# Optimization experiments

Hardware: AMD Instinct MI355X
Metric: run time of the kernel (lower is better)

## Reference

```python
import jax, jax.numpy as jnp
import numpy as np


def setup_inputs() -> dict:
    key = jax.random.key(0)
    k1, k2 = jax.random.split(key)
    q, k, d5 = 128, 2048, 768
    return {
        "tgt": jax.random.normal(k1, (q, d5), dtype=jnp.float32),
        "memory": jax.random.normal(k2, (k, d5), dtype=jnp.float32),
        "seq_len": 32,
    }


def reference(tgt, memory, seq_len):
    q, d5 = tgt.shape
    k, _ = memory.shape
    z = d5 // seq_len  # per-token sub-dim
    query_t = tgt.reshape(q, seq_len, z)    # [q, t, d]
    key_m = memory.reshape(k, seq_len, z)   # [k, s, d]
    # Full late-interaction similarity tensor [q, k, s, t]
    score = jnp.einsum('qtd,ksd->qkst', query_t, key_m)
    # max over memory tokens (s) and over query tokens (t), concat, mean
    pooled = jnp.concatenate((score.max(axis=2), score.max(axis=3)), axis=-1)  # [q, k, 2*seq_len]
    score_p = jax.nn.sigmoid(pooled.mean(axis=-1))  # [q, k]
    return (score_p, score_p)
```

## Files before the change

kernel.cpp:

```cpp
#include <hip/hip_runtime.h>
#include <hip/hip_bf16.h>

typedef __bf16 bf16x8 __attribute__((ext_vector_type(8)));
typedef float  f32x16 __attribute__((ext_vector_type(16)));

constexpr int QN  = 128;
constexpr int KN  = 2048;
constexpr int D5  = 768;
constexpr int SL  = 32;
constexpr int ZD  = 24;
constexpr int KCH = 16;

static __device__ __forceinline__ float max3f(float a, float b, float c) {
    return fmaxf(fmaxf(a, b), c);
}

static __device__ __forceinline__ float redmax16(const f32x16& a) {
    float x0 = max3f(a[0],  a[1],  a[2]);
    float x1 = max3f(a[3],  a[4],  a[5]);
    float x2 = max3f(a[6],  a[7],  a[8]);
    float x3 = max3f(a[9],  a[10], a[11]);
    float x4 = max3f(a[12], a[13], a[14]);
    float y0 = max3f(x0, x1, x2);
    float y1 = max3f(x3, x4, a[15]);
    return fmaxf(y0, y1);
}

__global__ __launch_bounds__(256, 4) void matcher_kernel(const float* __restrict__ tgt,
                                                         const float* __restrict__ mem,
                                                         float* __restrict__ out)
{
    __shared__ __align__(16) __bf16 Kf[KCH * 1024];

    const int tid = threadIdx.x;
    const int kc  = blockIdx.x;
    const int qg  = blockIdx.y;
    const int k0  = kc * KCH;

    for (int r = tid; r < KCH * SL; r += 256) {
        const int kl = r >> 5;
        const int s  = r & 31;
        const float* src = mem + (size_t)(k0 + kl) * D5 + s * ZD;
        float tv[24];
#pragma unroll
        for (int j = 0; j < 6; ++j) ((float4*)tv)[j] = ((const float4*)src)[j];
        bf16x8 a, b, c, z;
#pragma unroll
        for (int j = 0; j < 8; ++j) {
            a[j] = (__bf16)tv[j];
            b[j] = (__bf16)tv[8 + j];
            c[j] = (__bf16)tv[16 + j];
            z[j] = (__bf16)0.0f;
        }
        __bf16* base = Kf + kl * 1024;
        *(bf16x8*)(base +        s * 8)       = a;
        *(bf16x8*)(base + (32 +  s) * 8)      = b;
        *(bf16x8*)(base + 512 +  s * 8)       = c;
        *(bf16x8*)(base + 512 + (32 + s) * 8) = z;
    }

    const int lane = tid & 63;
    const int wv   = tid >> 6;
    const int t    = lane & 31;
    const int h    = lane >> 5;
    const int q    = qg * 4 + wv;

    const float4* p = (const float4*)(tgt + (size_t)q * D5 + t * ZD);
    bf16x8 aQ0, aQ1;
    {
        float4 u0 = p[2 * h], u1 = p[2 * h + 1];
        aQ0[0] = (__bf16)u0.x; aQ0[1] = (__bf16)u0.y; aQ0[2] = (__bf16)u0.z; aQ0[3] = (__bf16)u0.w;
        aQ0[4] = (__bf16)u1.x; aQ0[5] = (__bf16)u1.y; aQ0[6] = (__bf16)u1.z; aQ0[7] = (__bf16)u1.w;
        if (h == 0) {
            float4 w0 = p[4], w1 = p[5];
            aQ1[0] = (__bf16)w0.x; aQ1[1] = (__bf16)w0.y; aQ1[2] = (__bf16)w0.z; aQ1[3] = (__bf16)w0.w;
            aQ1[4] = (__bf16)w1.x; aQ1[5] = (__bf16)w1.y; aQ1[6] = (__bf16)w1.z; aQ1[7] = (__bf16)w1.w;
        } else {
#pragma unroll
            for (int j = 0; j < 8; ++j) aQ1[j] = (__bf16)0.0f;
        }
    }

    f32x16 zacc;
#pragma unroll
    for (int i = 0; i < 16; ++i) zacc[i] = 0.0f;

    __syncthreads();

    for (int kl = 0; kl < KCH; ++kl) {
        const __bf16* lb = Kf + kl * 1024 + lane * 8;
        bf16x8 bK0 = *(const bf16x8*)lb;
        bf16x8 bK1 = *(const bf16x8*)(lb + 512);

        f32x16 accS = __builtin_amdgcn_mfma_f32_32x32x16_bf16(aQ0, bK0, zacc, 0, 0, 0);
        accS        = __builtin_amdgcn_mfma_f32_32x32x16_bf16(aQ1, bK1, accS, 0, 0, 0);
        f32x16 accT = __builtin_amdgcn_mfma_f32_32x32x16_bf16(bK0, aQ0, zacc, 0, 0, 0);
        accT        = __builtin_amdgcn_mfma_f32_32x32x16_bf16(bK1, aQ1, accT, 0, 0, 0);

        float m1 = redmax16(accS);
        float m2 = redmax16(accT);
        m1 = fmaxf(m1, __shfl_xor(m1, 32));
        m2 = fmaxf(m2, __shfl_xor(m2, 32));

        float v = m1 + m2;
        v += __shfl_xor(v, 1);
        v += __shfl_xor(v, 2);
        v += __shfl_xor(v, 4);
        v += __shfl_xor(v, 8);
        v += __shfl_xor(v, 16);

        float r = 1.0f / (1.0f + __expf(-v * (1.0f / 64.0f)));
        if (lane == 0) {
            const int idx = q * KN + k0 + kl;
            out[idx] = r;
            out[idx + QN * KN] = r;
        }
    }
}

extern "C" void kernel_launch(void* const* d_in, const int* in_sizes, int n_in,
                              void* d_out, int out_size, void* d_ws, size_t ws_size,
                              hipStream_t stream)
{
    const float* tgt = (const float*)d_in[0];
    const float* mem = (const float*)d_in[1];
    float* out = (float*)d_out;
    dim3 grid(KN / KCH, QN / 4);
    matcher_kernel<<<grid, 256, 0, stream>>>(tgt, mem, out);
}
```

Before: 103.9 us.

## Defer per-key sum reduction to an LDS transpose pass and drop zero padding

Result: faster. 97.12 us (-6.5%).

```diff
diff --git a/kernel.cpp b/kernel.cpp
--- a/kernel.cpp
+++ b/kernel.cpp
@@ -30,7 +30,8 @@
                                                          const float* __restrict__ mem,
                                                          float* __restrict__ out)
 {
-    __shared__ __align__(16) __bf16 Kf[KCH * 1024];
+    __shared__ __align__(16) __bf16 Kf[KCH * 768];
+    __shared__ float vbuf[4][KCH * 32];
 
     const int tid = threadIdx.x;
     const int kc  = blockIdx.x;
@@ -44,19 +45,17 @@
         float tv[24];
 #pragma unroll
         for (int j = 0; j < 6; ++j) ((float4*)tv)[j] = ((const float4*)src)[j];
-        bf16x8 a, b, c, z;
+        bf16x8 a, b, c;
 #pragma unroll
         for (int j = 0; j < 8; ++j) {
             a[j] = (__bf16)tv[j];
             b[j] = (__bf16)tv[8 + j];
             c[j] = (__bf16)tv[16 + j];
-            z[j] = (__bf16)0.0f;
         }
-        __bf16* base = Kf + kl * 1024;
-        *(bf16x8*)(base +        s * 8)       = a;
-        *(bf16x8*)(base + (32 +  s) * 8)      = b;
-        *(bf16x8*)(base + 512 +  s * 8)       = c;
-        *(bf16x8*)(base + 512 + (32 + s) * 8) = z;
+        __bf16* base = Kf + kl * 768;
+        *(bf16x8*)(base +        s * 8)  = a;
+        *(bf16x8*)(base + (32 +  s) * 8) = b;
+        *(bf16x8*)(base + 512 +  s * 8)  = c;
     }
 
     const int lane = tid & 63;
@@ -65,14 +64,14 @@
     const int h    = lane >> 5;
     const int q    = qg * 4 + wv;
 
-    const float4* p = (const float4*)(tgt + (size_t)q * D5 + t * ZD);
+    const float4* p4 = (const float4*)(tgt + (size_t)q * D5 + t * ZD);
     bf16x8 aQ0, aQ1;
     {
-        float4 u0 = p[2 * h], u1 = p[2 * h + 1];
+        float4 u0 = p4[2 * h], u1 = p4[2 * h + 1];
         aQ0[0] = (__bf16)u0.x; aQ0[1] = (__bf16)u0.y; aQ0[2] = (__bf16)u0.z; aQ0[3] = (__bf16)u0.w;
         aQ0[4] = (__bf16)u1.x; aQ0[5] = (__bf16)u1.y; aQ0[6] = (__bf16)u1.z; aQ0[7] = (__bf16)u1.w;
         if (h == 0) {
-            float4 w0 = p[4], w1 = p[5];
+            float4 w0 = p4[4], w1 = p4[5];
             aQ1[0] = (__bf16)w0.x; aQ1[1] = (__bf16)w0.y; aQ1[2] = (__bf16)w0.z; aQ1[3] = (__bf16)w0.w;
             aQ1[4] = (__bf16)w1.x; aQ1[5] = (__bf16)w1.y; aQ1[6] = (__bf16)w1.z; aQ1[7] = (__bf16)w1.w;
         } else {
@@ -87,10 +86,16 @@
 
     __syncthreads();
 
+    float* vb = vbuf[wv];
+
+#pragma unroll
     for (int kl = 0; kl < KCH; ++kl) {
-        const __bf16* lb = Kf + kl * 1024 + lane * 8;
-        bf16x8 bK0 = *(const bf16x8*)lb;
-        bf16x8 bK1 = *(const bf16x8*)(lb + 512);
+        const __bf16* lb = Kf + kl * 768;
+        bf16x8 bK0 = *(const bf16x8*)(lb + lane * 8);
+        bf16x8 bK1;
+#pragma unroll
+        for (int j = 0; j < 8; ++j) bK1[j] = (__bf16)0.0f;
+        if (h == 0) bK1 = *(const bf16x8*)(lb + 512 + t * 8);
 
         f32x16 accS = __builtin_amdgcn_mfma_f32_32x32x16_bf16(aQ0, bK0, zacc, 0, 0, 0);
         accS        = __builtin_amdgcn_mfma_f32_32x32x16_bf16(aQ1, bK1, accS, 0, 0, 0);
@@ -101,17 +106,26 @@
         float m2 = redmax16(accT);
         m1 = fmaxf(m1, __shfl_xor(m1, 32));
         m2 = fmaxf(m2, __shfl_xor(m2, 32));
+        float v = m1 + m2;
+        if (h == 0) vb[(kl << 5) + (t ^ kl)] = v;
+    }
 
-        float v = m1 + m2;
-        v += __shfl_xor(v, 1);
-        v += __shfl_xor(v, 2);
-        v += __shfl_xor(v, 4);
-        v += __shfl_xor(v, 8);
-        v += __shfl_xor(v, 16);
-
-        float r = 1.0f / (1.0f + __expf(-v * (1.0f / 64.0f)));
-        if (lane == 0) {
-            const int idx = q * KN + k0 + kl;
+    {
+        const int p    = lane & 15;
+        const int half = (lane >> 4) & 1;
+        float x[16];
+#pragma unroll
+        for (int i = 0; i < 16; ++i)
+            x[i] = vb[(p << 5) + ((half << 4) + i ^ p)];
+        float s0 = (x[0] + x[1]) + (x[2] + x[3]);
+        float s1 = (x[4] + x[5]) + (x[6] + x[7]);
+        float s2 = (x[8] + x[9]) + (x[10] + x[11]);
+        float s3 = (x[12] + x[13]) + (x[14] + x[15]);
+        float sum = (s0 + s1) + (s2 + s3);
+        sum += __shfl_xor(sum, 16);
+        float r = 1.0f / (1.0f + __expf(-sum * (1.0f / 64.0f)));
+        if (lane < 16) {
+            const int idx = q * KN + k0 + p;
             out[idx] = r;
             out[idx + QN * KN] = r;
         }
```
